# Performance work log

Hardware: AMD Instinct MI355X
Metric: run time of the kernel (lower is better)

The kernel has to match this reference:

```python
import jax, jax.numpy as jnp
import numpy as np
import math

B, S, H, NH, NKV = 4, 2048, 2048, 16, 8
HD = H // NH           # 128
N_REP = NH // NKV      # 2


def rotate_half(t):
    t1, t2 = jnp.split(t, 2, axis=-1)
    return jnp.concatenate([-t2, t1], axis=-1)


def setup_inputs() -> dict:
    key = jax.random.key(0)
    ks = jax.random.split(key, 6)
    x = jax.random.normal(ks[0], (B, S, H), dtype=jnp.float32)
    # realistic RoPE tables [max_pos, head_dim]
    inv_freq = 1.0 / (10000.0 ** (np.arange(0, HD, 2, dtype=np.float32) / HD))
    t = np.arange(S, dtype=np.float32)
    freqs = np.outer(t, inv_freq)                 # [S, HD/2]
    emb = np.concatenate([freqs, freqs], axis=-1)  # [S, HD]
    cos = jnp.asarray(np.cos(emb), dtype=jnp.float32)
    sin = jnp.asarray(np.sin(emb), dtype=jnp.float32)
    sc = 0.02
    Wq = jax.random.normal(ks[1], (H, NH * HD), dtype=jnp.float32) * sc
    Wk = jax.random.normal(ks[2], (H, NKV * HD), dtype=jnp.float32) * sc
    Wv = jax.random.normal(ks[3], (H, NKV * HD), dtype=jnp.float32) * sc
    Wo = jax.random.normal(ks[4], (NH * HD, H), dtype=jnp.float32) * sc
    return {"x": x, "cos": cos, "sin": sin, "Wq": Wq, "Wk": Wk, "Wv": Wv, "Wo": Wo}


def reference(x, cos, sin, Wq, Wk, Wv, Wo):
    bsz, seq_len, _ = x.shape
    xq = (x @ Wq).reshape(bsz, seq_len, NH, HD)
    xk = (x @ Wk).reshape(bsz, seq_len, NKV, HD)
    xv = (x @ Wv).reshape(bsz, seq_len, NKV, HD)

    # RoPE (past_len = 0, no cache)
    c = cos[:seq_len][None, :, None, :]   # [1,S,1,HD]
    s = sin[:seq_len][None, :, None, :]
    xq = xq * c + rotate_half(xq) * s
    xk = xk * c + rotate_half(xk) * s

    # repeat_kv (GQA): [B,S,NKV,HD] -> [B,S,NH,HD]
    xk = jnp.repeat(xk, N_REP, axis=2)
    xv = jnp.repeat(xv, N_REP, axis=2)

    q = xq.transpose(0, 2, 1, 3)  # [B,NH,S,HD]
    k = xk.transpose(0, 2, 1, 3)
    v = xv.transpose(0, 2, 1, 3)

    scores = jnp.einsum('bhqd,bhkd->bhqk', q, k) / math.sqrt(HD)
    causal = jnp.triu(jnp.full((seq_len, seq_len), -jnp.inf, dtype=scores.dtype), k=1)
    scores = scores + causal[None, None]
    probs = jax.nn.softmax(scores.astype(jnp.float32), axis=-1).astype(q.dtype)
    out = jnp.einsum('bhqk,bhkd->bhqd', probs, v)
    out = out.transpose(0, 2, 1, 3).reshape(bsz, seq_len, NH * HD)
    return out @ Wo
```

## Files before the change

### kernel.cpp

```cpp
#include <hip/hip_runtime.h>
#include <stdint.h>

using bf16   = __bf16;
using bf16x4 = __attribute__((ext_vector_type(4))) __bf16;
using bf16x8 = __attribute__((ext_vector_type(8))) __bf16;
using f32x4  = __attribute__((ext_vector_type(4))) float;

#define DEV_INLINE __device__ __forceinline__

DEV_INLINE void gload16(const void* g, const void* l) {
  __builtin_amdgcn_global_load_lds(
      (const __attribute__((address_space(1))) unsigned int*)(uintptr_t)g,
      (__attribute__((address_space(3))) unsigned int*)(unsigned int)(uintptr_t)l,
      16, 0, 0);
}

DEV_INLINE f32x4 mfma16(bf16x8 a, bf16x8 b, f32x4 c) {
  return __builtin_amdgcn_mfma_f32_16x16x32_bf16(a, b, c, 0, 0, 0);
}

#define WAIT_LGKM0() do { \
  asm volatile("s_waitcnt lgkmcnt(0)" ::: "memory"); \
  __builtin_amdgcn_sched_barrier(0); } while (0)

__global__ void cast_f32_bf16(const float4* __restrict__ in, bf16* __restrict__ out, int n4) {
  int i = blockIdx.x * 256 + threadIdx.x;
  if (i >= n4) return;
  float4 v = in[i];
  bf16x4 o = { (bf16)v.x, (bf16)v.y, (bf16)v.z, (bf16)v.w };
  *(bf16x4*)(out + (size_t)i * 4) = o;
}

__global__ void transpose_cast(const float* __restrict__ in, bf16* __restrict__ out,
                               int rows, int cols) {
  __shared__ float tile[32][33];
  int c0 = blockIdx.x * 32, r0 = blockIdx.y * 32;
  int t = threadIdx.x, tc = t & 31, tr = t >> 5;
  for (int i = 0; i < 4; ++i)
    tile[tr + i*8][tc] = in[(size_t)(r0 + tr + i*8) * cols + (c0 + tc)];
  __syncthreads();
  for (int i = 0; i < 4; ++i)
    out[(size_t)(c0 + tr + i*8) * rows + (r0 + tc)] = (bf16)tile[tc][tr + i*8];
}


DEV_INLINE void stage_half(const bf16* __restrict__ src, int K, int k0, bf16* slot,
                           int w, int lr, int lc) {
#pragma unroll
  for (int i = 0; i < 2; ++i)
    gload16(src + (size_t)(w*16 + lr) * K + (k0 + i*32 + lc*8), slot + (w*2 + i) * 512);
}

DEV_INLINE void load_afr(bf16x8 (&af)[4][2], const bf16* slot, int wr2, int l) {
#pragma unroll
  for (int mi = 0; mi < 4; ++mi)
#pragma unroll
    for (int ks = 0; ks < 2; ++ks)
      af[mi][ks] = *(const bf16x8*)(slot + ((wr2*4 + mi)*2 + ks) * 512 + l*8);
}

template<bool PERM>
DEV_INLINE void load_bfr(bf16x8 (&bfr)[2][2], const bf16* slot, int wc2, int l) {
#pragma unroll
  for (int ni = 0; ni < 2; ++ni)
#pragma unroll
    for (int ks = 0; ks < 2; ++ks) {
      int mt = PERM ? (ni*4 + wc2) : (wc2*2 + ni);
      bfr[ni][ks] = *(const bf16x8*)(slot + (mt*2 + ks) * 512 + l*8);
    }
}

DEV_INLINE void mfma_quad(f32x4 (&aq)[4][2], const bf16x8 (&af)[4][2],
                          const bf16x8 (&bfr)[2][2]) {
#pragma unroll
  for (int mi = 0; mi < 4; ++mi)
#pragma unroll
    for (int ni = 0; ni < 2; ++ni)
#pragma unroll
      for (int ks = 0; ks < 2; ++ks)
        aq[mi][ni] = mfma16(af[mi][ks], bfr[ni][ks], aq[mi][ni]);
}

template<bool PERM, int K, int NK>
DEV_INLINE void gemm256_core(const bf16* __restrict__ A, const bf16* __restrict__ Bt,
                             int bm0, int bn0, bf16* sA, bf16* sB,
                             int w, int l, int lr, int lc, int wr2, int wc2,
                             f32x4 (&acc)[2][2][4][2]) {
  const bf16* Ar0 = A  + (size_t)bm0 * K;
  const bf16* Ar1 = Ar0 + (size_t)128 * K;
  const bf16* Br0 = Bt + (size_t)bn0 * K;
  const bf16* Br1 = Br0 + (size_t)128 * K;
  stage_half(Ar0, K, 0,  sA + 0*8192, w, lr, lc);
  stage_half(Br1, K, 0,  sB + 1*8192, w, lr, lc);
  stage_half(Ar1, K, 0,  sA + 1*8192, w, lr, lc);
  stage_half(Br0, K, 0,  sB + 0*8192, w, lr, lc);
  stage_half(Ar0, K, 64, sA + 2*8192, w, lr, lc);
  stage_half(Br1, K, 64, sB + 3*8192, w, lr, lc);
  __syncthreads();

  for (int kt = 0; kt < NK; ++kt) {
    const int k1 = (kt + 1 < NK ? kt + 1 : 0) * 64;
    const int k2 = (kt + 2 < NK ? kt + 2 : 0) * 64;
    bf16* A0s = sA + ((2*kt    ) & 3) * 8192;
    bf16* A1s = sA + ((2*kt + 1) & 3) * 8192;
    bf16* B0s = sB + ((2*kt    ) & 3) * 8192;
    bf16* B1s = sB + ((2*kt + 1) & 3) * 8192;
    bf16x8 af[4][2], bfr[2][2];

    load_afr(af, A0s, wr2, l);
    load_bfr<PERM>(bfr, B0s, wc2, l);
    stage_half(Ar1, K, k1, sA + ((2*kt + 3) & 3) * 8192, w, lr, lc);
    __builtin_amdgcn_s_barrier();
    WAIT_LGKM0();
    __builtin_amdgcn_s_setprio(1);
    mfma_quad(acc[0][0], af, bfr);
    __builtin_amdgcn_s_setprio(0);
    __builtin_amdgcn_s_barrier();

    load_bfr<PERM>(bfr, B1s, wc2, l);
    stage_half(Br0, K, k1, sB + ((2*kt + 2) & 3) * 8192, w, lr, lc);
    __builtin_amdgcn_s_barrier();
    WAIT_LGKM0();
    __builtin_amdgcn_s_setprio(1);
    mfma_quad(acc[0][1], af, bfr);
    __builtin_amdgcn_s_setprio(0);
    __builtin_amdgcn_s_barrier();

    load_afr(af, A1s, wr2, l);
    stage_half(Ar0, K, k2, sA + ((2*kt + 4) & 3) * 8192, w, lr, lc);
    __builtin_amdgcn_s_barrier();
    WAIT_LGKM0();
    __builtin_amdgcn_s_setprio(1);
    mfma_quad(acc[1][1], af, bfr);
    __builtin_amdgcn_s_setprio(0);
    __builtin_amdgcn_s_barrier();

    load_bfr<PERM>(bfr, B0s, wc2, l);
    stage_half(Br1, K, k2, sB + ((2*kt + 5) & 3) * 8192, w, lr, lc);
    __builtin_amdgcn_s_barrier();
    WAIT_LGKM0();
    __builtin_amdgcn_s_setprio(1);
    mfma_quad(acc[1][0], af, bfr);
    __builtin_amdgcn_s_setprio(0);
    asm volatile("s_waitcnt vmcnt(4)" ::: "memory");
    __builtin_amdgcn_sched_barrier(0);
    __builtin_amdgcn_s_barrier();
  }
  asm volatile("s_waitcnt vmcnt(0)" ::: "memory");
}

__global__ __launch_bounds__(512, 2)
void gemm256_rope(const bf16* __restrict__ A, const bf16* __restrict__ Bt,
                  const float* __restrict__ cs, const float* __restrict__ sn,
                  bf16* __restrict__ Qr, bf16* __restrict__ Kr,
                  bf16* __restrict__ Vbuf) {
  __shared__ bf16 sA[4 * 8192];
  __shared__ bf16 sB[4 * 8192];
  int id = blockIdx.x;
  int swz = (id & 7) * 64 + (id >> 3);
  int tm = swz >> 4, tn = swz & 15;
  int bm0 = tm * 256, bn0 = tn * 256;
  int tid = threadIdx.x, w = tid >> 6, l = tid & 63, lr = l & 15, lc = l >> 4;
  int wr2 = w >> 2, wc2 = w & 3;
  f32x4 acc[2][2][4][2] = {};
  gemm256_core<true, 2048, 32>(A, Bt, bm0, bn0, sA, sB, w, l, lr, lc, wr2, wc2, acc);

  int bb = bm0 >> 11, s0 = bm0 & 2047;
  int dlo = wc2 * 16 + lr;
#pragma unroll
  for (int nh = 0; nh < 2; ++nh) {
    int h128 = tn * 2 + nh;
    if (h128 < 24) {
      const float scale = (h128 < 16) ? 0.08838834764831845f * 1.4426950408889634f : 1.0f;
      bf16* dstB = (h128 < 16)
          ? Qr + (size_t)(bb * 16 + h128) * 2048 * 128
          : Kr + (size_t)(bb * 8 + (h128 - 16)) * 2048 * 128;
#pragma unroll
      for (int mh = 0; mh < 2; ++mh)
#pragma unroll
        for (int mi = 0; mi < 4; ++mi)
#pragma unroll
          for (int r = 0; r < 4; ++r) {
            int sl = s0 + mh*128 + wr2*64 + mi*16 + lc*4 + r;
            float c  = cs[sl * 128 + dlo];
            float sv = sn[sl * 128 + dlo];
            float lo = acc[mh][nh][mi][0][r], hi = acc[mh][nh][mi][1][r];
            bf16* dst = dstB + (size_t)sl * 128 + dlo;
            dst[0]  = (bf16)((lo * c - hi * sv) * scale);
            dst[64] = (bf16)((hi * c + lo * sv) * scale);
          }
    } else {
      int kvh = h128 - 24;
#pragma unroll
      for (int mh = 0; mh < 2; ++mh)
#pragma unroll
        for (int mi = 0; mi < 4; ++mi)
#pragma unroll
          for (int r = 0; r < 4; ++r) {
            int sl = s0 + mh*128 + wr2*64 + mi*16 + lc*4 + r;
            bf16* dst = Vbuf + ((size_t)(bb * 2048) + sl) * 1024 + kvh * 128 + dlo;
            dst[0]  = (bf16)acc[mh][nh][mi][0][r];
            dst[64] = (bf16)acc[mh][nh][mi][1][r];
          }
    }
  }
}

__global__ __launch_bounds__(512, 2)
void gemm256_out(const bf16* __restrict__ A, const bf16* __restrict__ Bt,
                 float* __restrict__ C) {
  __shared__ bf16 sA[4 * 8192];
  __shared__ bf16 sB[4 * 8192];
  int id = blockIdx.x;
  int swz = (id & 7) * 32 + (id >> 3);
  int tm = swz >> 3, tn = swz & 7;
  int bm0 = tm * 256, bn0 = tn * 256;
  int tid = threadIdx.x, w = tid >> 6, l = tid & 63, lr = l & 15, lc = l >> 4;
  int wr2 = w >> 2, wc2 = w & 3;
  f32x4 acc[2][2][4][2] = {};
  gemm256_core<false, 2048, 32>(A, Bt, bm0, bn0, sA, sB, w, l, lr, lc, wr2, wc2, acc);
#pragma unroll
  for (int mh = 0; mh < 2; ++mh)
#pragma unroll
    for (int nh = 0; nh < 2; ++nh)
#pragma unroll
      for (int mi = 0; mi < 4; ++mi)
#pragma unroll
        for (int ni = 0; ni < 2; ++ni)
#pragma unroll
          for (int r = 0; r < 4; ++r) {
            int row = bm0 + mh*128 + wr2*64 + mi*16 + lc*4 + r;
            int col = bn0 + nh*128 + wc2*32 + ni*16 + lr;
            C[(size_t)row * 2048 + col] = acc[mh][nh][mi][ni][r];
          }
}

__global__ void v_transpose(const bf16* __restrict__ Vbuf, bf16* __restrict__ Vt) {
  __shared__ bf16 tile[32][33];
  int s0 = blockIdx.x * 32, d0 = blockIdx.y * 32, bh = blockIdx.z;
  int b = bh >> 3, h = bh & 7;
  int t = threadIdx.x, tc = t & 31, tr = t >> 5;
  for (int i = 0; i < 4; ++i)
    tile[tr + i*8][tc] =
        Vbuf[((size_t)(b*2048) + s0 + tr + i*8) * 1024 + h*128 + d0 + tc];
  __syncthreads();
  for (int i = 0; i < 4; ++i)
    Vt[((size_t)bh * 128 + d0 + tr + i*8) * 2048 + s0 + tc] = tile[tc][tr + i*8];
}

__global__ __launch_bounds__(256, 2)
void attn_kernel(const bf16* __restrict__ Q, const bf16* __restrict__ Kg,
                 const bf16* __restrict__ Vt, bf16* __restrict__ Og) {
  __shared__ bf16 sK[32 * 512];
  __shared__ bf16 sV[32 * 512];
  int x = blockIdx.x, y = blockIdx.y;
  int qi = (x + y) & 31;
  int bkv = y;
  int b = bkv >> 3, kvh = bkv & 7;
  int tid = threadIdx.x, w = tid >> 6, l = tid & 63, lr = l & 15, lc = l >> 4;
  const bf16* Qb0 = Q + ((size_t)(b*16 + kvh*2) * 2048 + qi*64) * 128;
  const bf16* Qb1 = Qb0 + (size_t)2048 * 128;
  const bf16* Kb  = Kg + (size_t)bkv * 2048 * 128;
  const bf16* Vb  = Vt + (size_t)bkv * 128 * 2048;
  bf16x8 qf0[4], qf1[4];
  for (int ks = 0; ks < 4; ++ks) {
    size_t off = (size_t)(w*16 + lr) * 128 + ks*32 + lc*8;
    qf0[ks] = *(const bf16x8*)(Qb0 + off);
    qf1[ks] = *(const bf16x8*)(Qb1 + off);
  }
  f32x4 o0[8] = {}, o1[8] = {};
  float l0[4] = {0.f,0.f,0.f,0.f}, l1[4] = {0.f,0.f,0.f,0.f};
  int qrow = qi*64 + w*16 + lc*4;
  bf16* sP0 = sK + w * 2048;
  bf16* sP1 = sK + 8192 + w * 2048;
  int tmax = (qi + 2) >> 1;
  for (int t = 0; t < tmax; ++t) {
    __syncthreads();
    for (int i = 0; i < 8; ++i) {
      int id = w*8 + i;
      int nt = id >> 2, ks = id & 3;
      gload16(Kb + (size_t)(t*128 + nt*16 + lr) * 128 + ks*32 + lc*8, sK + id*512);
      gload16(Vb + (size_t)(nt*16 + lr) * 2048 + t*128 + ks*32 + lc*8, sV + id*512);
    }
    __syncthreads();
    f32x4 s0[8] = {}, s1[8] = {};
    for (int nt = 0; nt < 8; ++nt)
      for (int ks = 0; ks < 4; ++ks) {
        bf16x8 kf = *(const bf16x8*)(sK + (nt*4 + ks)*512 + l*8);
        s0[nt] = mfma16(qf0[ks], kf, s0[nt]);
        s1[nt] = mfma16(qf1[ks], kf, s1[nt]);
      }
    if (t == tmax - 1) {
      for (int nt = 0; nt < 8; ++nt) {
        int col = t*128 + nt*16 + lr;
        for (int r = 0; r < 4; ++r)
          if (col > qrow + r) { s0[nt][r] = -1e30f; s1[nt][r] = -1e30f; }
      }
    }
    __syncthreads();
    for (int nt = 0; nt < 8; ++nt) {
      int hi6 = (nt >> 2) * 1024;
      int blk = (nt*2 + (lr >> 3)) & 7;
      int off = lr & 7;
      for (int r = 0; r < 4; ++r) {
        int q = lc*4 + r;
        int addr = hi6 + q*64 + ((blk ^ (q & 7)) * 8) + off;
        float p0 = __builtin_amdgcn_exp2f(s0[nt][r]);
        float p1 = __builtin_amdgcn_exp2f(s1[nt][r]);
        l0[r] += p0;
        l1[r] += p1;
        sP0[addr] = (bf16)p0;
        sP1[addr] = (bf16)p1;
      }
    }
    asm volatile("s_waitcnt lgkmcnt(0)" ::: "memory");
    __builtin_amdgcn_sched_barrier(0);
    bf16x8 pf0[4], pf1[4];
    for (int ks = 0; ks < 4; ++ks) {
      int ra = (ks >> 1)*1024 + lr*64 + ((((ks & 1)*4 + lc) ^ (lr & 7)) * 8);
      pf0[ks] = *(const bf16x8*)(sP0 + ra);
      pf1[ks] = *(const bf16x8*)(sP1 + ra);
    }
    for (int nt = 0; nt < 8; ++nt)
      for (int ks = 0; ks < 4; ++ks) {
        bf16x8 vf = *(const bf16x8*)(sV + (nt*4 + ks)*512 + l*8);
        o0[nt] = mfma16(pf0[ks], vf, o0[nt]);
        o1[nt] = mfma16(pf1[ks], vf, o1[nt]);
      }
  }
  for (int msk = 1; msk < 16; msk <<= 1)
    for (int r = 0; r < 4; ++r) {
      l0[r] += __shfl_xor(l0[r], msk, 64);
      l1[r] += __shfl_xor(l1[r], msk, 64);
    }
  for (int r = 0; r < 4; ++r) {
    float inv0 = 1.f / l0[r];
    float inv1 = 1.f / l1[r];
    size_t row = (size_t)(b*2048) + qi*64 + w*16 + lc*4 + r;
    size_t base0 = row * 2048 + (kvh*2) * 128;
    for (int nt = 0; nt < 8; ++nt) {
      Og[base0 + nt*16 + lr]       = (bf16)(o0[nt][r] * inv0);
      Og[base0 + 128 + nt*16 + lr] = (bf16)(o1[nt][r] * inv1);
    }
  }
}

extern "C" void kernel_launch(void* const* d_in, const int* in_sizes, int n_in,
                              void* d_out, int out_size, void* d_ws, size_t ws_size,
                              hipStream_t stream) {
  (void)in_sizes; (void)n_in; (void)out_size; (void)ws_size;
  const float* x  = (const float*)d_in[0];
  const float* cs = (const float*)d_in[1];
  const float* sn = (const float*)d_in[2];
  const float* Wq = (const float*)d_in[3];
  const float* Wk = (const float*)d_in[4];
  const float* Wv = (const float*)d_in[5];
  const float* Wo = (const float*)d_in[6];
  float* out = (float*)d_out;

  char* p = (char*)d_ws;
  bf16* xb    = (bf16*)p;  p += (size_t)8192*2048*2;
  bf16* Wt    = (bf16*)p;  p += (size_t)4096*2048*2;
  bf16* Wot   = (bf16*)p;  p += (size_t)2048*2048*2;
  bf16* Qr    = (bf16*)p;  p += (size_t)64*2048*128*2;
  bf16* Kr    = (bf16*)p;  p += (size_t)32*2048*128*2;
  bf16* Vbuf  = (bf16*)p;  p += (size_t)8192*1024*2;
  bf16* Vtb   = (bf16*)p;  p += (size_t)32*2048*128*2;
  bf16* attnb = (bf16*)p;  p += (size_t)8192*2048*2;

  cast_f32_bf16<<<4194304/256, 256, 0, stream>>>((const float4*)x, xb, 4194304);
  transpose_cast<<<dim3(64,64), 256, 0, stream>>>(Wq, Wt, 2048, 2048);
  transpose_cast<<<dim3(32,64), 256, 0, stream>>>(Wk, Wt + (size_t)2048*2048, 2048, 1024);
  transpose_cast<<<dim3(32,64), 256, 0, stream>>>(Wv, Wt + (size_t)3072*2048, 2048, 1024);
  transpose_cast<<<dim3(64,64), 256, 0, stream>>>(Wo, Wot, 2048, 2048);
  gemm256_rope<<<dim3(512), 512, 0, stream>>>(xb, Wt, cs, sn, Qr, Kr, Vbuf);
  v_transpose<<<dim3(64,4,32), 256, 0, stream>>>(Vbuf, Vtb);
  attn_kernel<<<dim3(32,32), 256, 0, stream>>>(Qr, Kr, Vtb, attnb);
  gemm256_out<<<dim3(256), 512, 0, stream>>>(attnb, Wot, out);
}
```

Baseline: 541.7 us.

## Register-prefetch next K/V tile during QK compute in attention loop

Replaces the direct global-to-LDS loads of each K/V tile with register staging. The next tile is loaded into registers during the current tile's QK^T and softmax work, then written to LDS at the top of the next iteration. __syncthreads is replaced by raw s_barrier calls with explicit waitcnt and sched_barrier fences. This is meant to hide global-load latency behind MFMA work, at the cost of 16 extra bf16x8 registers per thread, which may reduce occupancy.

```diff
diff --git a/kernel.cpp b/kernel.cpp
--- a/kernel.cpp
+++ b/kernel.cpp
@@ -21,6 +21,11 @@
 
 #define WAIT_LGKM0() do { \
   asm volatile("s_waitcnt lgkmcnt(0)" ::: "memory"); \
+  __builtin_amdgcn_sched_barrier(0); } while (0)
+
+#define RAW_BARRIER() do { \
+  __builtin_amdgcn_sched_barrier(0); \
+  __builtin_amdgcn_s_barrier(); \
   __builtin_amdgcn_sched_barrier(0); } while (0)
 
 __global__ void cast_f32_bf16(const float4* __restrict__ in, bf16* __restrict__ out, int n4) {
@@ -274,15 +279,26 @@
   bf16* sP0 = sK + w * 2048;
   bf16* sP1 = sK + 8192 + w * 2048;
   int tmax = (qi + 2) >> 1;
+
+  bf16x8 kst[8], vst[8];
+#pragma unroll
+  for (int i = 0; i < 8; ++i) {
+    int id = w*8 + i, nt = id >> 2, ks = id & 3;
+    kst[i] = *(const bf16x8*)(Kb + (size_t)(nt*16 + lr) * 128 + ks*32 + lc*8);
+    vst[i] = *(const bf16x8*)(Vb + (size_t)(nt*16 + lr) * 2048 + ks*32 + lc*8);
+  }
+
   for (int t = 0; t < tmax; ++t) {
-    __syncthreads();
+    asm volatile("s_waitcnt vmcnt(0)" ::: "memory");
+    RAW_BARRIER();
+#pragma unroll
     for (int i = 0; i < 8; ++i) {
       int id = w*8 + i;
-      int nt = id >> 2, ks = id & 3;
-      gload16(Kb + (size_t)(t*128 + nt*16 + lr) * 128 + ks*32 + lc*8, sK + id*512);
-      gload16(Vb + (size_t)(nt*16 + lr) * 2048 + t*128 + ks*32 + lc*8, sV + id*512);
-    }
-    __syncthreads();
+      *(bf16x8*)(sK + id*512 + l*8) = kst[i];
+      *(bf16x8*)(sV + id*512 + l*8) = vst[i];
+    }
+    WAIT_LGKM0();
+    RAW_BARRIER();
     f32x4 s0[8] = {}, s1[8] = {};
     for (int nt = 0; nt < 8; ++nt)
       for (int ks = 0; ks < 4; ++ks) {
@@ -290,6 +306,14 @@
         s0[nt] = mfma16(qf0[ks], kf, s0[nt]);
         s1[nt] = mfma16(qf1[ks], kf, s1[nt]);
       }
+    if (t + 1 < tmax) {
+#pragma unroll
+      for (int i = 0; i < 8; ++i) {
+        int id = w*8 + i, nt = id >> 2, ks = id & 3;
+        kst[i] = *(const bf16x8*)(Kb + (size_t)((t+1)*128 + nt*16 + lr) * 128 + ks*32 + lc*8);
+        vst[i] = *(const bf16x8*)(Vb + (size_t)(nt*16 + lr) * 2048 + (t+1)*128 + ks*32 + lc*8);
+      }
+    }
     if (t == tmax - 1) {
       for (int nt = 0; nt < 8; ++nt) {
         int col = t*128 + nt*16 + lr;
@@ -297,7 +321,8 @@
           if (col > qrow + r) { s0[nt][r] = -1e30f; s1[nt][r] = -1e30f; }
       }
     }
-    __syncthreads();
+    WAIT_LGKM0();
+    RAW_BARRIER();
     for (int nt = 0; nt < 8; ++nt) {
       int hi6 = (nt >> 2) * 1024;
       int blk = (nt*2 + (lr >> 3)) & 7;
@@ -313,8 +338,7 @@
         sP1[addr] = (bf16)p1;
       }
     }
-    asm volatile("s_waitcnt lgkmcnt(0)" ::: "memory");
-    __builtin_amdgcn_sched_barrier(0);
+    WAIT_LGKM0();
     bf16x8 pf0[4], pf1[4];
     for (int ks = 0; ks < 4; ++ks) {
       int ra = (ks >> 1)*1024 + lr*64 + ((((ks & 1)*4 + lc) ^ (lr & 7)) * 8);
@@ -327,6 +351,7 @@
         o0[nt] = mfma16(pf0[ks], vf, o0[nt]);
         o1[nt] = mfma16(pf1[ks], vf, o1[nt]);
       }
+    WAIT_LGKM0();
   }
   for (int msk = 1; msk < 16; msk <<= 1)
     for (int r = 0; r < 4; ++r) {
```

After: 617.6 us. +14.0%, slower.
